# Kernel tuning notes

Hardware: AMD Instinct MI355X
Metric: run time of the kernel (lower is better)

Reference implementation:

```python
import jax, jax.numpy as jnp
import numpy as np
from jax import lax

B, D, H, STEPS = 16384, 256, 256, 25


def setup_inputs() -> dict:
    key = jax.random.key(0)
    k1, k2, k3, k4 = jax.random.split(key, 4)
    s1 = 1.0 / np.sqrt(D)
    s2 = 1.0 / np.sqrt(H)
    return {
        "z0": jax.random.normal(k1, (B, D), dtype=jnp.float32),
        "t_range": jnp.linspace(0.0, 1.0, STEPS, dtype=jnp.float32),
        "W1": jax.random.normal(k2, (D, H), dtype=jnp.float32) * s1,
        "b1": jnp.zeros((H,), dtype=jnp.float32),
        "wt": jax.random.normal(k3, (H,), dtype=jnp.float32) * 0.1,
        "W2": jax.random.normal(k4, (H, D), dtype=jnp.float32) * s2,
        "b2": jnp.zeros((D,), dtype=jnp.float32),
    }


def reference(z0, t_range, W1, b1, wt, W2, b2):
    # Euler solver: zt <- zt + dt * f(zt, t) for every t in t_range
    # (matches euler_solver: note it steps at ALL 25 grid points, incl. t_end)
    dt = t_range[1] - t_range[0]

    def dynamics(z, t):
        h = jnp.tanh(z @ W1 + b1 + t * wt)  # [B, H]
        return h @ W2 + b2                   # [B, D]

    def step(z, t):
        return z + dt * dynamics(z, t), None

    zT, _ = lax.scan(step, z0, t_range)
    return zT
```

## Files before the change

### kernel.cpp

```cpp
#include <hip/hip_runtime.h>

typedef short bf16x8 __attribute__((ext_vector_type(8)));
typedef float f32x4  __attribute__((ext_vector_type(4)));

#define NSTEP 25
#define SROW  264
#define LDSB  (32 * SROW)

__device__ __forceinline__ unsigned short f2bf(float x) {
    union { float f; unsigned int u; } v; v.f = x;
    unsigned int r = v.u + 0x7FFFu + ((v.u >> 16) & 1u);
    return (unsigned short)(r >> 16);
}

#if __has_builtin(__builtin_amdgcn_cvt_pk_bf16_f32)
typedef __bf16 bfv2 __attribute__((ext_vector_type(2)));
__device__ __forceinline__ unsigned int pk2bf(float a, float b) {
    union { bfv2 v; unsigned int u; } c;
    c.v = __builtin_amdgcn_cvt_pk_bf16_f32(a, b);
    return c.u;
}
#else
__device__ __forceinline__ unsigned int pk2bf(float a, float b) {
    return (unsigned int)f2bf(a) | ((unsigned int)f2bf(b) << 16);
}
#endif

__device__ __forceinline__ float tanh_fast(float x) {
    float e = __expf(2.0f * x);
    return 1.0f - 2.0f * __builtin_amdgcn_rcpf(e + 1.0f);
}

__global__ void prep_weights(const float* __restrict__ W1,
                             const float* __restrict__ W2,
                             unsigned short* __restrict__ Wr)
{
    int b = blockIdx.x;
    const float* src = (b < 256) ? W1 : W2;
    unsigned short* dst = Wr + ((b < 256) ? 0 : 65536);
    int idx = (b & 255) * 256 + threadIdx.x;
    int j  = idx & 7;
    int q  = (idx >> 3) & 3;
    int n  = (idx >> 5) & 255;
    int kc = idx >> 13;
    int p  = kc * 32 + q * 8 + j;
    int k  = (p & ~31) | ((p & 1) << 4) | ((p >> 1) & 15);
    dst[idx] = f2bf(src[k * 256 + n]);
}

__global__ void prep_w21(const float* __restrict__ W1,
                         const float* __restrict__ W2,
                         const float* __restrict__ b2,
                         const float* __restrict__ t_range,
                         unsigned short* __restrict__ W21r,
                         float* __restrict__ c1)
{
    __shared__ float row[256];
    int i = blockIdx.x, j = threadIdx.x;
    row[j] = (i < 256) ? W2[i * 256 + j] : b2[j];
    __syncthreads();
    float acc = 0.f;
    for (int d = 0; d < 256; ++d)
        acc = fmaf(row[d], W1[d * 256 + j], acc);
    if (i < 256) {
        float dt = t_range[1] - t_range[0];
        int p  = (i & ~31) | ((i & 15) << 1) | ((i >> 4) & 1);
        int kc = p >> 5, q = (p >> 3) & 3, jj = p & 7;
        W21r[kc * 8192 + j * 32 + q * 8 + jj] = f2bf(dt * acc);
    } else {
        c1[j] = acc;
    }
}

__global__ __launch_bounds__(256, 2) void ode_main(
    const float* __restrict__ z0,
    const float* __restrict__ t_range,
    const float* __restrict__ b1,
    const float* __restrict__ wt,
    const float* __restrict__ b2,
    const unsigned short* __restrict__ W1r,
    const unsigned short* __restrict__ W2r,
    const unsigned short* __restrict__ W21r,
    const float* __restrict__ c1,
    float* __restrict__ out)
{
    __shared__ __align__(16) unsigned short As[2 * LDSB];

    const int tid  = threadIdx.x;
    const int wave = tid >> 6;
    const int lane = tid & 63;
    const int q    = lane >> 4;
    const int l15  = lane & 15;
    const int row0 = blockIdx.x * 32;
    const int n0   = wave * 64;

    const float dt = t_range[1] - t_range[0];

    float bt[4], dbt[4];
#pragma unroll
    for (int tt = 0; tt < 4; ++tt) {
        int n = n0 + tt * 16 + l15;
        bt[tt]  = b1[n];
        dbt[tt] = dt * (wt[n] + c1[n]);
    }

#pragma unroll
    for (int band = 0; band < 2; ++band)
#pragma unroll
        for (int r = 0; r < 4; ++r) {
            int m = band * 16 + q * 4 + r;
            const float* zr = &z0[(row0 + m) * 256 + n0];
            *(unsigned int*)&As[m * SROW + n0 + l15 * 2] =
                pk2bf(zr[l15], zr[16 + l15]);
            *(unsigned int*)&As[m * SROW + n0 + 32 + l15 * 2] =
                pk2bf(zr[32 + l15], zr[48 + l15]);
        }
    __syncthreads();

    f32x4 y[2][4];
#pragma unroll
    for (int band = 0; band < 2; ++band)
#pragma unroll
        for (int tt = 0; tt < 4; ++tt) y[band][tt] = f32x4{0.f, 0.f, 0.f, 0.f};
#pragma unroll
    for (int kc = 0; kc < 8; ++kc) {
        bf16x8 a[2];
#pragma unroll
        for (int band = 0; band < 2; ++band)
            a[band] = *(const bf16x8*)&As[(band * 16 + l15) * SROW + kc * 32 + q * 8];
#pragma unroll
        for (int tt = 0; tt < 4; ++tt) {
            bf16x8 bb = *(const bf16x8*)&W1r[kc * 8192 + (n0 + tt * 16 + l15) * 32 + q * 8];
#pragma unroll
            for (int band = 0; band < 2; ++band)
                y[band][tt] = __builtin_amdgcn_mfma_f32_16x16x32_bf16(
                    a[band], bb, y[band][tt], 0, 0, 0);
        }
    }

    bf16x8 w21f[8][4];
#pragma unroll
    for (int kc = 0; kc < 8; ++kc)
#pragma unroll
        for (int tt = 0; tt < 4; ++tt)
            w21f[kc][tt] = *(const bf16x8*)&W21r[kc * 8192 + (n0 + tt * 16 + l15) * 32 + q * 8];

    f32x4 S[2][4];
#pragma unroll
    for (int band = 0; band < 2; ++band)
#pragma unroll
        for (int tt = 0; tt < 4; ++tt) S[band][tt] = f32x4{0.f, 0.f, 0.f, 0.f};

    for (int s = 0; s < NSTEP - 1; ++s) {
        const int buf = ((s + 1) & 1) * LDSB;
#pragma unroll
        for (int band = 0; band < 2; ++band)
#pragma unroll
            for (int r = 0; r < 4; ++r) {
                int m = band * 16 + q * 4 + r;
                float h0 = tanh_fast(y[band][0][r] + bt[0]);
                float h1 = tanh_fast(y[band][1][r] + bt[1]);
                float h2 = tanh_fast(y[band][2][r] + bt[2]);
                float h3 = tanh_fast(y[band][3][r] + bt[3]);
                S[band][0][r] += h0; S[band][1][r] += h1;
                S[band][2][r] += h2; S[band][3][r] += h3;
                *(unsigned int*)&As[buf + m * SROW + n0 + l15 * 2]      = pk2bf(h0, h1);
                *(unsigned int*)&As[buf + m * SROW + n0 + 32 + l15 * 2] = pk2bf(h2, h3);
            }
        __syncthreads();

#pragma unroll
        for (int kc = 0; kc < 8; ++kc) {
            bf16x8 a[2];
#pragma unroll
            for (int band = 0; band < 2; ++band)
                a[band] = *(const bf16x8*)&As[buf + (band * 16 + l15) * SROW + kc * 32 + q * 8];
#pragma unroll
            for (int band = 0; band < 2; ++band)
#pragma unroll
                for (int tt = 0; tt < 4; ++tt)
                    y[band][tt] = __builtin_amdgcn_mfma_f32_16x16x32_bf16(
                        a[band], w21f[kc][tt], y[band][tt], 0, 0, 0);
        }

#pragma unroll
        for (int tt = 0; tt < 4; ++tt) bt[tt] += dbt[tt];
    }

#pragma unroll
    for (int band = 0; band < 2; ++band)
#pragma unroll
        for (int r = 0; r < 4; ++r)
#pragma unroll
            for (int tt = 0; tt < 4; ++tt)
                S[band][tt][r] += tanh_fast(y[band][tt][r] + bt[tt]);

    {
        const int buf = LDSB;
#pragma unroll
        for (int band = 0; band < 2; ++band)
#pragma unroll
            for (int r = 0; r < 4; ++r) {
                int m = band * 16 + q * 4 + r;
                *(unsigned int*)&As[buf + m * SROW + n0 + l15 * 2] =
                    pk2bf(S[band][0][r], S[band][1][r]);
                *(unsigned int*)&As[buf + m * SROW + n0 + 32 + l15 * 2] =
                    pk2bf(S[band][2][r], S[band][3][r]);
            }
        __syncthreads();

        f32x4 acc[2][4];
#pragma unroll
        for (int band = 0; band < 2; ++band)
#pragma unroll
            for (int tt = 0; tt < 4; ++tt) acc[band][tt] = f32x4{0.f, 0.f, 0.f, 0.f};
#pragma unroll
        for (int kc = 0; kc < 8; ++kc) {
            bf16x8 a[2];
#pragma unroll
            for (int band = 0; band < 2; ++band)
                a[band] = *(const bf16x8*)&As[buf + (band * 16 + l15) * SROW + kc * 32 + q * 8];
#pragma unroll
            for (int tt = 0; tt < 4; ++tt) {
                bf16x8 bb = *(const bf16x8*)&W2r[kc * 8192 + (n0 + tt * 16 + l15) * 32 + q * 8];
#pragma unroll
                for (int band = 0; band < 2; ++band)
                    acc[band][tt] = __builtin_amdgcn_mfma_f32_16x16x32_bf16(
                        a[band], bb, acc[band][tt], 0, 0, 0);
            }
        }

        const float cb2 = (float)NSTEP * dt;
#pragma unroll
        for (int band = 0; band < 2; ++band)
#pragma unroll
            for (int tt = 0; tt < 4; ++tt) {
                float b2v = b2[n0 + tt * 16 + l15];
#pragma unroll
                for (int r = 0; r < 4; ++r) {
                    int idx = (row0 + band * 16 + q * 4 + r) * 256 + n0 + tt * 16 + l15;
                    out[idx] = z0[idx] + dt * acc[band][tt][r] + cb2 * b2v;
                }
            }
    }
}

extern "C" void kernel_launch(void* const* d_in, const int* in_sizes, int n_in,
                              void* d_out, int out_size, void* d_ws, size_t ws_size,
                              hipStream_t stream) {
    const float* z0      = (const float*)d_in[0];
    const float* t_range = (const float*)d_in[1];
    const float* W1      = (const float*)d_in[2];
    const float* b1      = (const float*)d_in[3];
    const float* wt      = (const float*)d_in[4];
    const float* W2      = (const float*)d_in[5];
    const float* b2      = (const float*)d_in[6];

    unsigned short* Wr = (unsigned short*)d_ws;
    unsigned short* W1r  = Wr;
    unsigned short* W2r  = Wr + 65536;
    unsigned short* W21r = Wr + 131072;
    float*          c1   = (float*)(Wr + 196608);

    prep_weights<<<512, 256, 0, stream>>>(W1, W2, Wr);
    prep_w21<<<257, 256, 0, stream>>>(W1, W2, b2, t_range, W21r, c1);
    ode_main<<<512, 256, 0, stream>>>(z0, t_range, b1, wt, b2,
                                      W1r, W2r, W21r, c1, (float*)d_out);
}
```

Baseline: 158.2 us.

## Merge weight prep kernels and split main kernel across eight waves per block

Folds the two weight-preparation kernels into one launch, which removes a kernel launch and its gap, and rewrites the W1/W2 reorder to index by source row. The main ODE kernel now runs 512 threads per block, with each of 8 waves owning 32 output columns instead of 64. That halves the per-wave accumulators and cached W21 fragments, lowering register pressure so more waves can hide tanh and MFMA latency. In exchange each block pays more barrier participants, and the A operand is read from LDS by twice as many waves.

```diff
diff --git a/kernel.cpp b/kernel.cpp
--- a/kernel.cpp
+++ b/kernel.cpp
@@ -31,48 +31,43 @@
     return 1.0f - 2.0f * __builtin_amdgcn_rcpf(e + 1.0f);
 }
 
-__global__ void prep_weights(const float* __restrict__ W1,
-                             const float* __restrict__ W2,
-                             unsigned short* __restrict__ Wr)
-{
-    int b = blockIdx.x;
-    const float* src = (b < 256) ? W1 : W2;
-    unsigned short* dst = Wr + ((b < 256) ? 0 : 65536);
-    int idx = (b & 255) * 256 + threadIdx.x;
-    int j  = idx & 7;
-    int q  = (idx >> 3) & 3;
-    int n  = (idx >> 5) & 255;
-    int kc = idx >> 13;
-    int p  = kc * 32 + q * 8 + j;
-    int k  = (p & ~31) | ((p & 1) << 4) | ((p >> 1) & 15);
-    dst[idx] = f2bf(src[k * 256 + n]);
-}
-
-__global__ void prep_w21(const float* __restrict__ W1,
+__global__ void prep_all(const float* __restrict__ W1,
                          const float* __restrict__ W2,
                          const float* __restrict__ b2,
                          const float* __restrict__ t_range,
+                         unsigned short* __restrict__ Wr,
                          unsigned short* __restrict__ W21r,
                          float* __restrict__ c1)
 {
     __shared__ float row[256];
-    int i = blockIdx.x, j = threadIdx.x;
-    row[j] = (i < 256) ? W2[i * 256 + j] : b2[j];
-    __syncthreads();
-    float acc = 0.f;
-    for (int d = 0; d < 256; ++d)
-        acc = fmaf(row[d], W1[d * 256 + j], acc);
-    if (i < 256) {
-        float dt = t_range[1] - t_range[0];
-        int p  = (i & ~31) | ((i & 15) << 1) | ((i >> 4) & 1);
-        int kc = p >> 5, q = (p >> 3) & 3, jj = p & 7;
-        W21r[kc * 8192 + j * 32 + q * 8 + jj] = f2bf(dt * acc);
+    int b = blockIdx.x;
+    if (b < 512) {
+        const float* src = (b < 256) ? W1 : W2;
+        unsigned short* dst = Wr + ((b < 256) ? 0 : 65536);
+        int k = b & 255;
+        int n = threadIdx.x;
+        int p  = (k & ~31) | ((k & 15) << 1) | ((k >> 4) & 1);
+        int kc = p >> 5, q = (p >> 3) & 3, j = p & 7;
+        dst[kc * 8192 + n * 32 + q * 8 + j] = f2bf(src[k * 256 + n]);
     } else {
-        c1[j] = acc;
-    }
-}
-
-__global__ __launch_bounds__(256, 2) void ode_main(
+        int i = b - 512, j = threadIdx.x;
+        row[j] = (i < 256) ? W2[i * 256 + j] : b2[j];
+        __syncthreads();
+        float acc = 0.f;
+        for (int d = 0; d < 256; ++d)
+            acc = fmaf(row[d], W1[d * 256 + j], acc);
+        if (i < 256) {
+            float dt = t_range[1] - t_range[0];
+            int p  = (i & ~31) | ((i & 15) << 1) | ((i >> 4) & 1);
+            int kc = p >> 5, q = (p >> 3) & 3, jj = p & 7;
+            W21r[kc * 8192 + j * 32 + q * 8 + jj] = f2bf(dt * acc);
+        } else {
+            c1[j] = acc;
+        }
+    }
+}
+
+__global__ __launch_bounds__(512, 4) void ode_main(
     const float* __restrict__ z0,
     const float* __restrict__ t_range,
     const float* __restrict__ b1,
@@ -92,13 +87,13 @@
     const int q    = lane >> 4;
     const int l15  = lane & 15;
     const int row0 = blockIdx.x * 32;
-    const int n0   = wave * 64;
+    const int n0   = wave * 32;
 
     const float dt = t_range[1] - t_range[0];
 
-    float bt[4], dbt[4];
-#pragma unroll
-    for (int tt = 0; tt < 4; ++tt) {
+    float bt[2], dbt[2];
+#pragma unroll
+    for (int tt = 0; tt < 2; ++tt) {
         int n = n0 + tt * 16 + l15;
         bt[tt]  = b1[n];
         dbt[tt] = dt * (wt[n] + c1[n]);
@@ -112,16 +107,14 @@
             const float* zr = &z0[(row0 + m) * 256 + n0];
             *(unsigned int*)&As[m * SROW + n0 + l15 * 2] =
                 pk2bf(zr[l15], zr[16 + l15]);
-            *(unsigned int*)&As[m * SROW + n0 + 32 + l15 * 2] =
-                pk2bf(zr[32 + l15], zr[48 + l15]);
         }
     __syncthreads();
 
-    f32x4 y[2][4];
-#pragma unroll
-    for (int band = 0; band < 2; ++band)
-#pragma unroll
-        for (int tt = 0; tt < 4; ++tt) y[band][tt] = f32x4{0.f, 0.f, 0.f, 0.f};
+    f32x4 y[2][2];
+#pragma unroll
+    for (int band = 0; band < 2; ++band)
+#pragma unroll
+        for (int tt = 0; tt < 2; ++tt) y[band][tt] = f32x4{0.f, 0.f, 0.f, 0.f};
 #pragma unroll
     for (int kc = 0; kc < 8; ++kc) {
         bf16x8 a[2];
@@ -129,7 +122,7 @@
         for (int band = 0; band < 2; ++band)
             a[band] = *(const bf16x8*)&As[(band * 16 + l15) * SROW + kc * 32 + q * 8];
 #pragma unroll
-        for (int tt = 0; tt < 4; ++tt) {
+        for (int tt = 0; tt < 2; ++tt) {
             bf16x8 bb = *(const bf16x8*)&W1r[kc * 8192 + (n0 + tt * 16 + l15) * 32 + q * 8];
 #pragma unroll
             for (int band = 0; band < 2; ++band)
@@ -138,18 +131,18 @@
         }
     }
 
-    bf16x8 w21f[8][4];
+    bf16x8 w21f[8][2];
 #pragma unroll
     for (int kc = 0; kc < 8; ++kc)
 #pragma unroll
-        for (int tt = 0; tt < 4; ++tt)
+        for (int tt = 0; tt < 2; ++tt)
             w21f[kc][tt] = *(const bf16x8*)&W21r[kc * 8192 + (n0 + tt * 16 + l15) * 32 + q * 8];
 
-    f32x4 S[2][4];
-#pragma unroll
-    for (int band = 0; band < 2; ++band)
-#pragma unroll
-        for (int tt = 0; tt < 4; ++tt) S[band][tt] = f32x4{0.f, 0.f, 0.f, 0.f};
+    f32x4 S[2][2];
+#pragma unroll
+    for (int band = 0; band < 2; ++band)
+#pragma unroll
+        for (int tt = 0; tt < 2; ++tt) S[band][tt] = f32x4{0.f, 0.f, 0.f, 0.f};
 
     for (int s = 0; s < NSTEP - 1; ++s) {
         const int buf = ((s + 1) & 1) * LDSB;
@@ -160,12 +153,8 @@
                 int m = band * 16 + q * 4 + r;
                 float h0 = tanh_fast(y[band][0][r] + bt[0]);
                 float h1 = tanh_fast(y[band][1][r] + bt[1]);
-                float h2 = tanh_fast(y[band][2][r] + bt[2]);
-                float h3 = tanh_fast(y[band][3][r] + bt[3]);
                 S[band][0][r] += h0; S[band][1][r] += h1;
-                S[band][2][r] += h2; S[band][3][r] += h3;
-                *(unsigned int*)&As[buf + m * SROW + n0 + l15 * 2]      = pk2bf(h0, h1);
-                *(unsigned int*)&As[buf + m * SROW + n0 + 32 + l15 * 2] = pk2bf(h2, h3);
+                *(unsigned int*)&As[buf + m * SROW + n0 + l15 * 2] = pk2bf(h0, h1);
             }
         __syncthreads();
 
@@ -178,13 +167,13 @@
 #pragma unroll
             for (int band = 0; band < 2; ++band)
 #pragma unroll
-                for (int tt = 0; tt < 4; ++tt)
+                for (int tt = 0; tt < 2; ++tt)
                     y[band][tt] = __builtin_amdgcn_mfma_f32_16x16x32_bf16(
                         a[band], w21f[kc][tt], y[band][tt], 0, 0, 0);
         }
 
 #pragma unroll
-        for (int tt = 0; tt < 4; ++tt) bt[tt] += dbt[tt];
+        for (int tt = 0; tt < 2; ++tt) bt[tt] += dbt[tt];
     }
 
 #pragma unroll
@@ -192,7 +181,7 @@
 #pragma unroll
         for (int r = 0; r < 4; ++r)
 #pragma unroll
-            for (int tt = 0; tt < 4; ++tt)
+            for (int tt = 0; tt < 2; ++tt)
                 S[band][tt][r] += tanh_fast(y[band][tt][r] + bt[tt]);
 
     {
@@ -204,16 +193,14 @@
                 int m = band * 16 + q * 4 + r;
                 *(unsigned int*)&As[buf + m * SROW + n0 + l15 * 2] =
                     pk2bf(S[band][0][r], S[band][1][r]);
-                *(unsigned int*)&As[buf + m * SROW + n0 + 32 + l15 * 2] =
-                    pk2bf(S[band][2][r], S[band][3][r]);
             }
         __syncthreads();
 
-        f32x4 acc[2][4];
-#pragma unroll
-        for (int band = 0; band < 2; ++band)
-#pragma unroll
-            for (int tt = 0; tt < 4; ++tt) acc[band][tt] = f32x4{0.f, 0.f, 0.f, 0.f};
+        f32x4 acc[2][2];
+#pragma unroll
+        for (int band = 0; band < 2; ++band)
+#pragma unroll
+            for (int tt = 0; tt < 2; ++tt) acc[band][tt] = f32x4{0.f, 0.f, 0.f, 0.f};
 #pragma unroll
         for (int kc = 0; kc < 8; ++kc) {
             bf16x8 a[2];
@@ -221,7 +208,7 @@
             for (int band = 0; band < 2; ++band)
                 a[band] = *(const bf16x8*)&As[buf + (band * 16 + l15) * SROW + kc * 32 + q * 8];
 #pragma unroll
-            for (int tt = 0; tt < 4; ++tt) {
+            for (int tt = 0; tt < 2; ++tt) {
                 bf16x8 bb = *(const bf16x8*)&W2r[kc * 8192 + (n0 + tt * 16 + l15) * 32 + q * 8];
 #pragma unroll
                 for (int band = 0; band < 2; ++band)
@@ -234,7 +221,7 @@
 #pragma unroll
         for (int band = 0; band < 2; ++band)
 #pragma unroll
-            for (int tt = 0; tt < 4; ++tt) {
+            for (int tt = 0; tt < 2; ++tt) {
                 float b2v = b2[n0 + tt * 16 + l15];
 #pragma unroll
                 for (int r = 0; r < 4; ++r) {
@@ -262,8 +249,7 @@
     unsigned short* W21r = Wr + 131072;
     float*          c1   = (float*)(Wr + 196608);
 
-    prep_weights<<<512, 256, 0, stream>>>(W1, W2, Wr);
-    prep_w21<<<257, 256, 0, stream>>>(W1, W2, b2, t_range, W21r, c1);
-    ode_main<<<512, 256, 0, stream>>>(z0, t_range, b1, wt, b2,
+    prep_all<<<769, 256, 0, stream>>>(W1, W2, b2, t_range, Wr, W21r, c1);
+    ode_main<<<512, 512, 0, stream>>>(z0, t_range, b1, wt, b2,
                                       W1r, W2r, W21r, c1, (float*)d_out);
 }
```

After: 152.9 us. 1.04x faster.
